# Optimization experiments

Hardware: AMD Instinct MI355X
Metric: run time of the kernel (lower is better)

Reference implementation:

```python
import jax, jax.numpy as jnp
import numpy as np

N_NODES = 100000
N_EDGES = 3200000
N_PAIRS = 500000
D_IN = 256
D_HID = 256
D_OUT = 2


def setup_inputs() -> dict:
    key = jax.random.key(0)
    ks = jax.random.split(key, 9)
    s1 = 1.0 / np.sqrt(D_IN)
    s2 = 1.0 / np.sqrt(D_HID)
    s3 = 1.0 / np.sqrt(2 * D_HID)
    return {
        "x": jax.random.normal(ks[0], (N_NODES, D_IN), jnp.float32),
        "edge_index": jax.random.randint(ks[1], (2, N_EDGES), 0, N_NODES, jnp.int64 if jax.config.jax_enable_x64 else jnp.int32),
        "index": jax.random.randint(ks[2], (N_PAIRS, 2), 0, N_NODES, jnp.int64 if jax.config.jax_enable_x64 else jnp.int32),
        "W1": jax.random.normal(ks[3], (D_HID, D_IN), jnp.float32) * s1,
        "b1": jnp.zeros((D_HID,), jnp.float32),
        "W2": jax.random.normal(ks[4], (D_HID, D_HID), jnp.float32) * s2,
        "b2": jnp.zeros((D_HID,), jnp.float32),
        "W3": jax.random.normal(ks[5], (D_OUT, 2 * D_HID), jnp.float32) * s3,
        "b3": jnp.zeros((D_OUT,), jnp.float32),
    }


def _gin_conv(x, edge_index, W, b):
    # PyG GINConv (eps=0): nn((1+eps)*x + sum_{j in N(i)} x_j)
    src, dst = edge_index[0], edge_index[1]
    agg = jax.ops.segment_sum(x[src], dst, num_segments=x.shape[0])  # [N, d]
    return (x + agg) @ W.T + b


def reference(x, edge_index, index, W1, b1, W2, b2, W3, b3):
    h = jax.nn.relu(_gin_conv(x, edge_index, W1, b1))   # [N, D_HID]
    h = jax.nn.relu(_gin_conv(h, edge_index, W2, b2))   # [N, D_HID]
    pair = jnp.concatenate((h[index[:, 0]], h[index[:, 1]]), axis=-1)  # [P, 2*D_HID]
    logits = pair @ W3.T + b3                            # [P, D_OUT]
    return jax.nn.log_softmax(logits, axis=1)
```

## Files before the change

kernel.cpp:

```cpp
#include <hip/hip_runtime.h>
#include <hip/hip_bf16.h>

constexpr int N_NODES = 100000;
constexpr int N_EDGES = 3200000;
constexpr int N_PAIRS = 500000;
constexpr int D       = 256;
constexpr int NRANGE  = 8;
constexpr int RSPAN   = 12500;
constexpr int SCANN   = 100352;

using frag_ab = __attribute__((ext_vector_type(8))) short;
using frag_cd = __attribute__((ext_vector_type(4))) float;
typedef unsigned short ushort8 __attribute__((ext_vector_type(8)));

static __device__ __forceinline__ float b2f(unsigned short u) {
  return __uint_as_float(((unsigned)u) << 16);
}
static __device__ __forceinline__ unsigned short f2bf(float f) {
  unsigned u = __float_as_uint(f);
  unsigned r = (u + 0x7fff + ((u >> 16) & 1)) >> 16;
  return (unsigned short)r;
}

__global__ void zero_ints(int* __restrict__ p, int n) {
  int i = blockIdx.x * blockDim.x + threadIdx.x;
  if (i < n) p[i] = 0;
}

__global__ void f32_to_bf16(const float4* __restrict__ in, ushort4* __restrict__ out, int n4) {
  int i = blockIdx.x * blockDim.x + threadIdx.x;
  int stride = gridDim.x * blockDim.x;
  for (; i < n4; i += stride) {
    const float4 v = in[i];
    ushort4 o;
    o.x = f2bf(v.x); o.y = f2bf(v.y); o.z = f2bf(v.z); o.w = f2bf(v.w);
    out[i] = o;
  }
}

__global__ void conv_weights(const float4* __restrict__ W1, const float4* __restrict__ W2,
                             ushort4* __restrict__ W1b, ushort4* __restrict__ W2b) {
  const int i = blockIdx.x * blockDim.x + threadIdx.x;
  const bool second = i >= 16384;
  const int k = second ? i - 16384 : i;
  if (k < 16384) {
    const float4 v = second ? W2[k] : W1[k];
    ushort4 o;
    o.x = f2bf(v.x); o.y = f2bf(v.y); o.z = f2bf(v.z); o.w = f2bf(v.w);
    if (second) W2b[k] = o; else W1b[k] = o;
  }
}

__global__ void hist_kernel(const int* __restrict__ ei, int* __restrict__ counts) {
  int i = blockIdx.x * blockDim.x + threadIdx.x;
  if (i < N_EDGES) atomicAdd(&counts[ei[N_EDGES + i]], 1);
}

__global__ __launch_bounds__(1024) void scan_block_k(const int* __restrict__ in,
                                                     int* __restrict__ out,
                                                     int* __restrict__ bsum) {
  __shared__ int wsum[16];
  const int t = threadIdx.x, lane = t & 63, w = t >> 6;
  const int gid = blockIdx.x * 1024 + t;
  const int v = in[gid];
  int s = v;
#pragma unroll
  for (int off = 1; off < 64; off <<= 1) {
    int u = __shfl_up(s, off, 64);
    if (lane >= off) s += u;
  }
  if (lane == 63) wsum[w] = s;
  __syncthreads();
  if (t < 16) {
    int ws = wsum[t];
#pragma unroll
    for (int off = 1; off < 16; off <<= 1) {
      int u = __shfl_up(ws, off, 64);
      if (lane >= off) ws += u;
    }
    wsum[t] = ws;
  }
  __syncthreads();
  const int wpre = (w == 0) ? 0 : wsum[w - 1];
  out[gid] = wpre + s - v;
  if (t == 1023) bsum[blockIdx.x] = wsum[15];
}

__global__ __launch_bounds__(1024) void scan_small(const int* __restrict__ in,
                                                   int* __restrict__ out, int n) {
  __shared__ int wsum[16];
  const int t = threadIdx.x, lane = t & 63, w = t >> 6;
  int v = (t < n) ? in[t] : 0;
  int s = v;
#pragma unroll
  for (int off = 1; off < 64; off <<= 1) {
    int u = __shfl_up(s, off, 64);
    if (lane >= off) s += u;
  }
  if (lane == 63) wsum[w] = s;
  __syncthreads();
  if (t < 16) {
    int ws = wsum[t];
#pragma unroll
    for (int off = 1; off < 16; off <<= 1) {
      int u = __shfl_up(ws, off, 64);
      if (lane >= off) ws += u;
    }
    wsum[t] = ws;
  }
  __syncthreads();
  const int wpre = (w == 0) ? 0 : wsum[w - 1];
  if (t < n) out[t] = wpre + s - v;
}

__global__ __launch_bounds__(1024) void scan_add_k(int* __restrict__ cursor,
                                                   int* __restrict__ pos,
                                                   const int* __restrict__ bsum2,
                                                   int* __restrict__ rc) {
  const int gid = blockIdx.x * 1024 + threadIdx.x;
  const int v = cursor[gid] + bsum2[gid >> 10];
  cursor[gid] = v;
  pos[gid] = v;
  if (gid < N_NODES && gid % RSPAN == 0) rc[gid / RSPAN] = v;
}

constexpr int PART_SEG = 4096;
__global__ __launch_bounds__(256) void partition_kernel(const int* __restrict__ ei,
                                                        int* __restrict__ rc,
                                                        int2* __restrict__ bucket) {
  __shared__ int lcnt[NRANGE];
  __shared__ int lbase[NRANGE];
  const int t = threadIdx.x;
  const int base = blockIdx.x * PART_SEG;
  if (t < NRANGE) lcnt[t] = 0;
  __syncthreads();

  int rnk[16], rng[16], sv[16], dv[16];
#pragma unroll
  for (int j = 0; j < 16; ++j) {
    const int i = base + j * 256 + t;
    if (i < N_EDGES) {
      sv[j] = ei[i];
      dv[j] = ei[N_EDGES + i];
      rng[j] = dv[j] / RSPAN;
      rnk[j] = atomicAdd(&lcnt[rng[j]], 1);
    } else rng[j] = -1;
  }
  __syncthreads();
  if (t < NRANGE) lbase[t] = atomicAdd(&rc[t], lcnt[t]);
  __syncthreads();
#pragma unroll
  for (int j = 0; j < 16; ++j) {
    if (rng[j] >= 0) {
      int2 e; e.x = sv[j]; e.y = dv[j];
      bucket[lbase[rng[j]] + rnk[j]] = e;
    }
  }
}

constexpr int FLB = 128;
__global__ __launch_bounds__(256) void fill_local(const int2* __restrict__ bucket,
                                                  const int* __restrict__ cursor,
                                                  int* __restrict__ pos,
                                                  int* __restrict__ csr) {
  const int r = blockIdx.x & 7;
  const int j = blockIdx.x >> 3;
  const int beg = cursor[(size_t)r * RSPAN];
  const int end = (r < 7) ? cursor[(size_t)(r + 1) * RSPAN] : N_EDGES;
  for (int i = beg + j * 256 + threadIdx.x; i < end; i += FLB * 256) {
    const int2 e = bucket[i];
    const int p = atomicAdd(&pos[e.y], 1);
    csr[p] = e.x;
  }
}

__global__ __launch_bounds__(256) void gather_agg_bf16(const ushort* __restrict__ x,
                                                       const int* __restrict__ csr,
                                                       const int* __restrict__ cursor,
                                                       const int* __restrict__ counts,
                                                       ushort* __restrict__ out) {
  const int node = blockIdx.x * 4 + (threadIdx.x >> 6);
  const int lane = threadIdx.x & 63;
  const int half = lane >> 5;
  const int fl   = lane & 31;
  if (node >= N_NODES) return;
  const int beg = cursor[node];
  const int end = beg + counts[node];
  const size_t fo = (size_t)fl * 8;

  float acc[8];
#pragma unroll
  for (int j = 0; j < 8; ++j) acc[j] = 0.f;

  if (half == 0) {
    const ushort8 self = *reinterpret_cast<const ushort8*>(x + (size_t)node * D + fo);
#pragma unroll
    for (int j = 0; j < 8; ++j) acc[j] += b2f(self[j]);
  }

  int o = beg + half;
  for (; o + 6 < end; o += 8) {
    const int s0 = csr[o], s1 = csr[o + 2], s2 = csr[o + 4], s3 = csr[o + 6];
    const ushort8 v0 = *reinterpret_cast<const ushort8*>(x + (size_t)s0 * D + fo);
    const ushort8 v1 = *reinterpret_cast<const ushort8*>(x + (size_t)s1 * D + fo);
    const ushort8 v2 = *reinterpret_cast<const ushort8*>(x + (size_t)s2 * D + fo);
    const ushort8 v3 = *reinterpret_cast<const ushort8*>(x + (size_t)s3 * D + fo);
#pragma unroll
    for (int j = 0; j < 8; ++j)
      acc[j] += (b2f(v0[j]) + b2f(v1[j])) + (b2f(v2[j]) + b2f(v3[j]));
  }
  for (; o < end; o += 2) {
    const ushort8 v = *reinterpret_cast<const ushort8*>(x + (size_t)csr[o] * D + fo);
#pragma unroll
    for (int j = 0; j < 8; ++j) acc[j] += b2f(v[j]);
  }

#pragma unroll
  for (int j = 0; j < 8; ++j) acc[j] += __shfl_xor(acc[j], 32, 64);

  if (half == 0) {
    ushort8 ov;
#pragma unroll
    for (int j = 0; j < 8; ++j) ov[j] = f2bf(acc[j]);
    *reinterpret_cast<ushort8*>(out + (size_t)node * D + fo) = ov;
  }
}

__global__ __launch_bounds__(256) void gemm_mfma_bf16(const ushort* __restrict__ A,
                                                      const ushort* __restrict__ W,
                                                      const float* __restrict__ bias,
                                                      ushort* __restrict__ C,
                                                      int M) {
  __shared__ __align__(16) ushort As[64 * 256];
  __shared__ __align__(16) ushort Ws[64 * 256];

  const int t = threadIdx.x;
  const int w = t >> 6, l = t & 63;
  const int row0 = blockIdx.x * 64;
  const int col0 = blockIdx.y * 64;

  {
    const float4 zero4 = {0.f, 0.f, 0.f, 0.f};
#pragma unroll
    for (int i = 0; i < 8; ++i) {
      const int chunk = t + i * 256;
      const int r  = chunk >> 5;
      const int kb = (chunk & 31) << 4;
      const int swz = kb ^ ((r & 7) << 4);
      const int grow = row0 + r;
      float4 av = zero4;
      if (grow < M)
        av = *reinterpret_cast<const float4*>(
            reinterpret_cast<const char*>(A) + (size_t)grow * 512 + kb);
      *reinterpret_cast<float4*>(reinterpret_cast<char*>(As) + r * 512 + swz) = av;
      const float4 wv = *reinterpret_cast<const float4*>(
          reinterpret_cast<const char*>(W) + (size_t)(col0 + r) * 512 + kb);
      *reinterpret_cast<float4*>(reinterpret_cast<char*>(Ws) + r * 512 + swz) = wv;
    }
  }
  __syncthreads();

  const int g  = l >> 4;
  const int fr = l & 15;

  frag_cd acc[4];
#pragma unroll
  for (int c = 0; c < 4; ++c) {
    acc[c][0] = 0.f; acc[c][1] = 0.f; acc[c][2] = 0.f; acc[c][3] = 0.f;
  }

  const int arow = w * 16 + fr;
  const char* Asb = reinterpret_cast<const char*>(As);
  const char* Wsb = reinterpret_cast<const char*>(Ws);
#pragma unroll
  for (int ks = 0; ks < 8; ++ks) {
    const int kb = ks * 64 + g * 16;
    const frag_ab af = *reinterpret_cast<const frag_ab*>(
        Asb + arow * 512 + (kb ^ ((arow & 7) << 4)));
#pragma unroll
    for (int c = 0; c < 4; ++c) {
      const int wrow = c * 16 + fr;
      const frag_ab bf = *reinterpret_cast<const frag_ab*>(
          Wsb + wrow * 512 + (kb ^ ((wrow & 7) << 4)));
      acc[c] = __builtin_amdgcn_mfma_f32_16x16x32_bf16(af, bf, acc[c], 0, 0, 0);
    }
  }
  __syncthreads();

  ushort* Ct = As;
#pragma unroll
  for (int c = 0; c < 4; ++c) {
    const int col = c * 16 + fr;
    const float bv = bias[col0 + col];
#pragma unroll
    for (int r = 0; r < 4; ++r) {
      const int rl = w * 16 + g * 4 + r;
      Ct[rl * 64 + col] = f2bf(fmaxf(acc[c][r] + bv, 0.f));
    }
  }
  __syncthreads();
#pragma unroll
  for (int i = 0; i < 2; ++i) {
    const int chunk = t + i * 256;
    const int r  = chunk >> 3;
    const int cb = (chunk & 7) << 4;
    const int grow = row0 + r;
    if (grow < M)
      *reinterpret_cast<float4*>(reinterpret_cast<char*>(C) + (size_t)grow * 512 + col0 * 2 + cb) =
          *reinterpret_cast<const float4*>(reinterpret_cast<const char*>(Ct) + r * 128 + cb);
  }
}

__global__ __launch_bounds__(256) void proj_kernel(const ushort* __restrict__ h,
                                                   const float* __restrict__ W3,
                                                   float4* __restrict__ proj) {
  const int node = blockIdx.x * 4 + (threadIdx.x >> 6);
  const int lane = threadIdx.x & 63;
  if (node >= N_NODES) return;

  const ushort4 hv = *reinterpret_cast<const ushort4*>(h + (size_t)node * D + lane * 4);
  const float h0 = b2f(hv.x), h1 = b2f(hv.y), h2 = b2f(hv.z), h3 = b2f(hv.w);

  const float4 wa0 = *reinterpret_cast<const float4*>(W3 + lane * 4);
  const float4 wa1 = *reinterpret_cast<const float4*>(W3 + 512 + lane * 4);
  const float4 wb0 = *reinterpret_cast<const float4*>(W3 + 256 + lane * 4);
  const float4 wb1 = *reinterpret_cast<const float4*>(W3 + 768 + lane * 4);

  float a0 = h0 * wa0.x + h1 * wa0.y + h2 * wa0.z + h3 * wa0.w;
  float a1 = h0 * wa1.x + h1 * wa1.y + h2 * wa1.z + h3 * wa1.w;
  float b0 = h0 * wb0.x + h1 * wb0.y + h2 * wb0.z + h3 * wb0.w;
  float b1 = h0 * wb1.x + h1 * wb1.y + h2 * wb1.z + h3 * wb1.w;

#pragma unroll
  for (int off = 32; off > 0; off >>= 1) {
    a0 += __shfl_xor(a0, off, 64);
    a1 += __shfl_xor(a1, off, 64);
    b0 += __shfl_xor(b0, off, 64);
    b1 += __shfl_xor(b1, off, 64);
  }
  if (lane == 0) {
    float4 o; o.x = a0; o.y = a1; o.z = b0; o.w = b1;
    proj[node] = o;
  }
}

__global__ __launch_bounds__(256) void pair_lite(const float4* __restrict__ proj,
                                                 const int* __restrict__ idx,
                                                 const float* __restrict__ b3,
                                                 float* __restrict__ out) {
  const int p = blockIdx.x * blockDim.x + threadIdx.x;
  if (p >= N_PAIRS) return;
  const int2 ii = reinterpret_cast<const int2*>(idx)[p];
  const float4 pa = proj[ii.x];
  const float4 pb = proj[ii.y];
  float l0 = pa.x + pb.z + b3[0];
  float l1 = pa.y + pb.w + b3[1];
  const float m = fmaxf(l0, l1);
  const float lse = m + logf(expf(l0 - m) + expf(l1 - m));
  float2 o; o.x = l0 - lse; o.y = l1 - lse;
  reinterpret_cast<float2*>(out)[p] = o;
}

extern "C" void kernel_launch(void* const* d_in, const int* in_sizes, int n_in,
                              void* d_out, int out_size, void* d_ws, size_t ws_size,
                              hipStream_t stream) {
  const float* x   = (const float*)d_in[0];
  const int*   ei  = (const int*)d_in[1];
  const int*   idx = (const int*)d_in[2];
  const float* W1  = (const float*)d_in[3];
  const float* b1  = (const float*)d_in[4];
  const float* W2  = (const float*)d_in[5];
  const float* b2  = (const float*)d_in[6];
  const float* W3  = (const float*)d_in[7];
  const float* b3  = (const float*)d_in[8];
  float* out = (float*)d_out;

  char* ws = (char*)d_ws;
  ushort* xb    = (ushort*)(ws);
  ushort* aggb  = (ushort*)(ws + 51200000);
  int2*   bucket= (int2*)(ws + 51200000);
  ushort* hb    = (ushort*)(ws + 102400000);
  ushort* W1b   = (ushort*)(ws + 153600000);
  ushort* W2b   = (ushort*)(ws + 153731072);
  int* counts   = (int*)(ws + 153862144);
  int* cursor   = (int*)(ws + 154263552);
  int* pos      = (int*)(ws + 154664960);
  int* csr      = (int*)(ws + 155066368);
  float4* proj  = (float4*)(ws + 167866368);
  int* bsum     = (int*)(ws + 169466368);
  int* bsum2    = (int*)(ws + 169466880);
  int* rc       = (int*)(ws + 169467392);

  const dim3 blk(256);
  const size_t feat = (size_t)N_NODES * D;
  constexpr int SCAN_BLOCKS = SCANN / 1024;
  const dim3 edgeGrid((N_EDGES + 255) / 256);
  const dim3 partGrid((N_EDGES + PART_SEG - 1) / PART_SEG);
  const dim3 flocGrid(NRANGE * FLB);
  const dim3 nodeGrid((N_NODES + 3) / 4);
  const dim3 gemmGrid((N_NODES + 63) / 64, D / 64);
  const dim3 pairGrid((N_PAIRS + 255) / 256);

  f32_to_bf16<<<dim3(4096), blk, 0, stream>>>((const float4*)x, (ushort4*)xb, (int)(feat / 4));
  conv_weights<<<dim3(128), blk, 0, stream>>>((const float4*)W1, (const float4*)W2,
                                              (ushort4*)W1b, (ushort4*)W2b);

  zero_ints<<<dim3((SCANN + 255) / 256), blk, 0, stream>>>(counts, SCANN);
  hist_kernel<<<edgeGrid, blk, 0, stream>>>(ei, counts);
  scan_block_k<<<dim3(SCAN_BLOCKS), dim3(1024), 0, stream>>>(counts, cursor, bsum);
  scan_small<<<1, 1024, 0, stream>>>(bsum, bsum2, SCAN_BLOCKS);
  scan_add_k<<<dim3(SCAN_BLOCKS), dim3(1024), 0, stream>>>(cursor, pos, bsum2, rc);
  partition_kernel<<<partGrid, blk, 0, stream>>>(ei, rc, bucket);
  fill_local<<<flocGrid, blk, 0, stream>>>(bucket, cursor, pos, csr);

  gather_agg_bf16<<<nodeGrid, blk, 0, stream>>>(xb, csr, cursor, counts, aggb);
  gemm_mfma_bf16<<<gemmGrid, blk, 0, stream>>>(aggb, W1b, b1, hb, N_NODES);

  gather_agg_bf16<<<nodeGrid, blk, 0, stream>>>(hb, csr, cursor, counts, aggb);
  gemm_mfma_bf16<<<gemmGrid, blk, 0, stream>>>(aggb, W2b, b2, hb, N_NODES);

  proj_kernel<<<nodeGrid, blk, 0, stream>>>(hb, W3, proj);
  pair_lite<<<pairGrid, blk, 0, stream>>>(proj, idx, b3, out);
}
```

Before: 915.9 us.

## Fuse conversions, pack bucket edges, and fold projection into second GEMM

Merges the x/W1/W2 bf16 conversions into one kernel and combines zeroing of counts and the projection buffer. Packs each bucketed edge into a single int (17-bit src plus local dst offset), halving partition and fill traffic. Swaps the GEMM grid axes so column tiles of a row block run adjacently. Drops the final h store and proj_kernel by having the second GEMM epilogue compute W3 partial dot products and atomically add them into proj. This adds float atomics, which make the summation order nondeterministic.

```diff
diff --git a/kernel.cpp b/kernel.cpp
--- a/kernel.cpp
+++ b/kernel.cpp
@@ -22,32 +22,27 @@
   return (unsigned short)r;
 }
 
-__global__ void zero_ints(int* __restrict__ p, int n) {
+__global__ void zero2_kernel(int* __restrict__ counts, int* __restrict__ projz) {
+  const int i = blockIdx.x * blockDim.x + threadIdx.x;
+  if (i < SCANN) counts[i] = 0;
+  const int j = i - SCANN;
+  if (j >= 0 && j < 4 * N_NODES) projz[j] = 0;
+}
+
+__global__ void conv_all(const float4* __restrict__ x, const float4* __restrict__ W1,
+                         const float4* __restrict__ W2, ushort4* __restrict__ xb,
+                         ushort4* __restrict__ W1b, ushort4* __restrict__ W2b, int n4x) {
+  const int total = n4x + 2 * 16384;
   int i = blockIdx.x * blockDim.x + threadIdx.x;
-  if (i < n) p[i] = 0;
-}
-
-__global__ void f32_to_bf16(const float4* __restrict__ in, ushort4* __restrict__ out, int n4) {
-  int i = blockIdx.x * blockDim.x + threadIdx.x;
-  int stride = gridDim.x * blockDim.x;
-  for (; i < n4; i += stride) {
-    const float4 v = in[i];
+  const int stride = gridDim.x * blockDim.x;
+  for (; i < total; i += stride) {
+    float4 v; ushort4* dst; int k;
+    if (i < n4x) { v = x[i]; dst = xb; k = i; }
+    else if (i < n4x + 16384) { k = i - n4x; v = W1[k]; dst = W1b; }
+    else { k = i - n4x - 16384; v = W2[k]; dst = W2b; }
     ushort4 o;
     o.x = f2bf(v.x); o.y = f2bf(v.y); o.z = f2bf(v.z); o.w = f2bf(v.w);
-    out[i] = o;
-  }
-}
-
-__global__ void conv_weights(const float4* __restrict__ W1, const float4* __restrict__ W2,
-                             ushort4* __restrict__ W1b, ushort4* __restrict__ W2b) {
-  const int i = blockIdx.x * blockDim.x + threadIdx.x;
-  const bool second = i >= 16384;
-  const int k = second ? i - 16384 : i;
-  if (k < 16384) {
-    const float4 v = second ? W2[k] : W1[k];
-    ushort4 o;
-    o.x = f2bf(v.x); o.y = f2bf(v.y); o.z = f2bf(v.z); o.w = f2bf(v.w);
-    if (second) W2b[k] = o; else W1b[k] = o;
+    dst[k] = o;
   }
 }
 
@@ -127,7 +122,7 @@
 constexpr int PART_SEG = 4096;
 __global__ __launch_bounds__(256) void partition_kernel(const int* __restrict__ ei,
                                                         int* __restrict__ rc,
-                                                        int2* __restrict__ bucket) {
+                                                        int* __restrict__ bucket) {
   __shared__ int lcnt[NRANGE];
   __shared__ int lbase[NRANGE];
   const int t = threadIdx.x;
@@ -135,14 +130,15 @@
   if (t < NRANGE) lcnt[t] = 0;
   __syncthreads();
 
-  int rnk[16], rng[16], sv[16], dv[16];
+  int rnk[16], rng[16], pv[16];
 #pragma unroll
   for (int j = 0; j < 16; ++j) {
     const int i = base + j * 256 + t;
     if (i < N_EDGES) {
-      sv[j] = ei[i];
-      dv[j] = ei[N_EDGES + i];
-      rng[j] = dv[j] / RSPAN;
+      const int sv = ei[i];
+      const int dv = ei[N_EDGES + i];
+      rng[j] = dv / RSPAN;
+      pv[j] = sv | ((dv - rng[j] * RSPAN) << 17);
       rnk[j] = atomicAdd(&lcnt[rng[j]], 1);
     } else rng[j] = -1;
   }
@@ -151,26 +147,26 @@
   __syncthreads();
 #pragma unroll
   for (int j = 0; j < 16; ++j) {
-    if (rng[j] >= 0) {
-      int2 e; e.x = sv[j]; e.y = dv[j];
-      bucket[lbase[rng[j]] + rnk[j]] = e;
-    }
+    if (rng[j] >= 0) bucket[lbase[rng[j]] + rnk[j]] = pv[j];
   }
 }
 
 constexpr int FLB = 128;
-__global__ __launch_bounds__(256) void fill_local(const int2* __restrict__ bucket,
+__global__ __launch_bounds__(256) void fill_local(const int* __restrict__ bucket,
                                                   const int* __restrict__ cursor,
                                                   int* __restrict__ pos,
                                                   int* __restrict__ csr) {
   const int r = blockIdx.x & 7;
   const int j = blockIdx.x >> 3;
-  const int beg = cursor[(size_t)r * RSPAN];
-  const int end = (r < 7) ? cursor[(size_t)(r + 1) * RSPAN] : N_EDGES;
+  const int rbase = r * RSPAN;
+  const int beg = cursor[(size_t)rbase];
+  const int end = (r < 7) ? cursor[(size_t)rbase + RSPAN] : N_EDGES;
   for (int i = beg + j * 256 + threadIdx.x; i < end; i += FLB * 256) {
-    const int2 e = bucket[i];
-    const int p = atomicAdd(&pos[e.y], 1);
-    csr[p] = e.x;
+    const int e = bucket[i];
+    const int src = e & 0x1FFFF;
+    const int dst = rbase + (e >> 17);
+    const int p = atomicAdd(&pos[dst], 1);
+    csr[p] = src;
   }
 }
 
@@ -226,18 +222,21 @@
   }
 }
 
-__global__ __launch_bounds__(256) void gemm_mfma_bf16(const ushort* __restrict__ A,
-                                                      const ushort* __restrict__ W,
-                                                      const float* __restrict__ bias,
-                                                      ushort* __restrict__ C,
-                                                      int M) {
+template <bool WRITE_C>
+__global__ __launch_bounds__(256) void gemm_mfma(const ushort* __restrict__ A,
+                                                 const ushort* __restrict__ W,
+                                                 const float* __restrict__ bias,
+                                                 ushort* __restrict__ C,
+                                                 const float* __restrict__ W3,
+                                                 float* __restrict__ proj,
+                                                 int M) {
   __shared__ __align__(16) ushort As[64 * 256];
   __shared__ __align__(16) ushort Ws[64 * 256];
 
   const int t = threadIdx.x;
   const int w = t >> 6, l = t & 63;
-  const int row0 = blockIdx.x * 64;
-  const int col0 = blockIdx.y * 64;
+  const int row0 = blockIdx.y * 64;
+  const int col0 = blockIdx.x * 64;
 
   {
     const float4 zero4 = {0.f, 0.f, 0.f, 0.f};
@@ -299,48 +298,39 @@
     }
   }
   __syncthreads();
-#pragma unroll
-  for (int i = 0; i < 2; ++i) {
-    const int chunk = t + i * 256;
-    const int r  = chunk >> 3;
-    const int cb = (chunk & 7) << 4;
+
+  if constexpr (WRITE_C) {
+#pragma unroll
+    for (int i = 0; i < 2; ++i) {
+      const int chunk = t + i * 256;
+      const int r  = chunk >> 3;
+      const int cb = (chunk & 7) << 4;
+      const int grow = row0 + r;
+      if (grow < M)
+        *reinterpret_cast<float4*>(reinterpret_cast<char*>(C) + (size_t)grow * 512 + col0 * 2 + cb) =
+            *reinterpret_cast<const float4*>(reinterpret_cast<const char*>(Ct) + r * 128 + cb);
+    }
+  } else {
+    const int r = t >> 2;
+    const int q = t & 3;
     const int grow = row0 + r;
-    if (grow < M)
-      *reinterpret_cast<float4*>(reinterpret_cast<char*>(C) + (size_t)grow * 512 + col0 * 2 + cb) =
-          *reinterpret_cast<const float4*>(reinterpret_cast<const char*>(Ct) + r * 128 + cb);
-  }
-}
-
-__global__ __launch_bounds__(256) void proj_kernel(const ushort* __restrict__ h,
-                                                   const float* __restrict__ W3,
-                                                   float4* __restrict__ proj) {
-  const int node = blockIdx.x * 4 + (threadIdx.x >> 6);
-  const int lane = threadIdx.x & 63;
-  if (node >= N_NODES) return;
-
-  const ushort4 hv = *reinterpret_cast<const ushort4*>(h + (size_t)node * D + lane * 4);
-  const float h0 = b2f(hv.x), h1 = b2f(hv.y), h2 = b2f(hv.z), h3 = b2f(hv.w);
-
-  const float4 wa0 = *reinterpret_cast<const float4*>(W3 + lane * 4);
-  const float4 wa1 = *reinterpret_cast<const float4*>(W3 + 512 + lane * 4);
-  const float4 wb0 = *reinterpret_cast<const float4*>(W3 + 256 + lane * 4);
-  const float4 wb1 = *reinterpret_cast<const float4*>(W3 + 768 + lane * 4);
-
-  float a0 = h0 * wa0.x + h1 * wa0.y + h2 * wa0.z + h3 * wa0.w;
-  float a1 = h0 * wa1.x + h1 * wa1.y + h2 * wa1.z + h3 * wa1.w;
-  float b0 = h0 * wb0.x + h1 * wb0.y + h2 * wb0.z + h3 * wb0.w;
-  float b1 = h0 * wb1.x + h1 * wb1.y + h2 * wb1.z + h3 * wb1.w;
-
-#pragma unroll
-  for (int off = 32; off > 0; off >>= 1) {
-    a0 += __shfl_xor(a0, off, 64);
-    a1 += __shfl_xor(a1, off, 64);
-    b0 += __shfl_xor(b0, off, 64);
-    b1 += __shfl_xor(b1, off, 64);
-  }
-  if (lane == 0) {
-    float4 o; o.x = a0; o.y = a1; o.z = b0; o.w = b1;
-    proj[node] = o;
+    if (grow < M) {
+      float pa0 = 0.f, pa1 = 0.f, pb0 = 0.f, pb1 = 0.f;
+      const int cb = q * 16;
+#pragma unroll
+      for (int j = 0; j < 16; ++j) {
+        const float hv = b2f(Ct[r * 64 + cb + j]);
+        const int gc = col0 + cb + j;
+        pa0 += hv * W3[gc];
+        pa1 += hv * W3[512 + gc];
+        pb0 += hv * W3[256 + gc];
+        pb1 += hv * W3[768 + gc];
+      }
+      atomicAdd(&proj[grow * 4 + 0], pa0);
+      atomicAdd(&proj[grow * 4 + 1], pa1);
+      atomicAdd(&proj[grow * 4 + 2], pb0);
+      atomicAdd(&proj[grow * 4 + 3], pb1);
+    }
   }
 }
 
@@ -378,7 +368,7 @@
   char* ws = (char*)d_ws;
   ushort* xb    = (ushort*)(ws);
   ushort* aggb  = (ushort*)(ws + 51200000);
-  int2*   bucket= (int2*)(ws + 51200000);
+  int*    bucket= (int*)(ws + 51200000);
   ushort* hb    = (ushort*)(ws + 102400000);
   ushort* W1b   = (ushort*)(ws + 153600000);
   ushort* W2b   = (ushort*)(ws + 153731072);
@@ -386,7 +376,7 @@
   int* cursor   = (int*)(ws + 154263552);
   int* pos      = (int*)(ws + 154664960);
   int* csr      = (int*)(ws + 155066368);
-  float4* proj  = (float4*)(ws + 167866368);
+  float* projf  = (float*)(ws + 167866368);
   int* bsum     = (int*)(ws + 169466368);
   int* bsum2    = (int*)(ws + 169466880);
   int* rc       = (int*)(ws + 169467392);
@@ -394,18 +384,19 @@
   const dim3 blk(256);
   const size_t feat = (size_t)N_NODES * D;
   constexpr int SCAN_BLOCKS = SCANN / 1024;
+  const dim3 zero2Grid((SCANN + 4 * N_NODES + 255) / 256);
   const dim3 edgeGrid((N_EDGES + 255) / 256);
   const dim3 partGrid((N_EDGES + PART_SEG - 1) / PART_SEG);
   const dim3 flocGrid(NRANGE * FLB);
   const dim3 nodeGrid((N_NODES + 3) / 4);
-  const dim3 gemmGrid((N_NODES + 63) / 64, D / 64);
+  const dim3 gemmGrid(D / 64, (N_NODES + 63) / 64);
   const dim3 pairGrid((N_PAIRS + 255) / 256);
 
-  f32_to_bf16<<<dim3(4096), blk, 0, stream>>>((const float4*)x, (ushort4*)xb, (int)(feat / 4));
-  conv_weights<<<dim3(128), blk, 0, stream>>>((const float4*)W1, (const float4*)W2,
-                                              (ushort4*)W1b, (ushort4*)W2b);
-
-  zero_ints<<<dim3((SCANN + 255) / 256), blk, 0, stream>>>(counts, SCANN);
+  conv_all<<<dim3(4096), blk, 0, stream>>>((const float4*)x, (const float4*)W1,
+                                           (const float4*)W2, (ushort4*)xb,
+                                           (ushort4*)W1b, (ushort4*)W2b, (int)(feat / 4));
+  zero2_kernel<<<zero2Grid, blk, 0, stream>>>(counts, (int*)projf);
+
   hist_kernel<<<edgeGrid, blk, 0, stream>>>(ei, counts);
   scan_block_k<<<dim3(SCAN_BLOCKS), dim3(1024), 0, stream>>>(counts, cursor, bsum);
   scan_small<<<1, 1024, 0, stream>>>(bsum, bsum2, SCAN_BLOCKS);
@@ -414,11 +405,10 @@
   fill_local<<<flocGrid, blk, 0, stream>>>(bucket, cursor, pos, csr);
 
   gather_agg_bf16<<<nodeGrid, blk, 0, stream>>>(xb, csr, cursor, counts, aggb);
-  gemm_mfma_bf16<<<gemmGrid, blk, 0, stream>>>(aggb, W1b, b1, hb, N_NODES);
+  gemm_mfma<true><<<gemmGrid, blk, 0, stream>>>(aggb, W1b, b1, hb, nullptr, nullptr, N_NODES);
 
   gather_agg_bf16<<<nodeGrid, blk, 0, stream>>>(hb, csr, cursor, counts, aggb);
-  gemm_mfma_bf16<<<gemmGrid, blk, 0, stream>>>(aggb, W2b, b2, hb, N_NODES);
-
-  proj_kernel<<<nodeGrid, blk, 0, stream>>>(hb, W3, proj);
-  pair_lite<<<pairGrid, blk, 0, stream>>>(proj, idx, b3, out);
-}
+  gemm_mfma<false><<<gemmGrid, blk, 0, stream>>>(aggb, W2b, b2, nullptr, W3, projf, N_NODES);
+
+  pair_lite<<<pairGrid, blk, 0, stream>>>((const float4*)projf, idx, b3, out);
+}
```

Result: slower. 1.368 ms (+49.4%).
